# Performance work log

Hardware: AMD Instinct MI355X
Metric: run time of the kernel (lower is better)

Reference implementation:

```python
import jax, jax.numpy as jnp
import numpy as np

B, N, M, G, F = 8, 1000, 64, 50, 128


def setup_inputs() -> dict:
    key = jax.random.key(0)
    ks = jax.random.split(key, 9)
    s = 0.05
    return {
        "features": jax.random.normal(ks[0], (B, N, F), jnp.float32),
        "rbf_expansion": jax.random.uniform(ks[1], (B, N, M, G), jnp.float32),
        "neighbor_list": jax.random.randint(ks[2], (B, N, M), 0, N, jnp.int64),
        "W_init": jax.random.normal(ks[3], (F, F), jnp.float32) * s,
        "W1": jax.random.normal(ks[4], (G, F), jnp.float32) * s,
        "b1": jnp.zeros((F,), jnp.float32),
        "W2": jax.random.normal(ks[5], (F, F), jnp.float32) * s,
        "b2": jnp.zeros((F,), jnp.float32),
        "nbr_w": jax.random.normal(ks[6], (F,), jnp.float32) * s,
        "Wo1": jax.random.normal(ks[7], (F, F), jnp.float32) * s,
        "bo1": jnp.zeros((F,), jnp.float32),
        "Wo2": jax.random.normal(ks[8], (F, F), jnp.float32) * s,
        "bo2": jnp.zeros((F,), jnp.float32),
    }


def reference(features, rbf_expansion, neighbor_list, W_init, W1, b1, W2, b2,
              nbr_w, Wo1, bo1, Wo2, bo2):
    b, n, m = neighbor_list.shape
    # 1. atom-wise linear, no bias/activation: [B,N,F]
    init = features @ W_init
    # 2. CFConv: filter generator on RBF expansion -> [B,N,M,F]
    filt = jnp.tanh(rbf_expansion @ W1 + b1) @ W2 + b2
    # gather neighbor features: init[b, neighbor_list[b,n,m], :] -> [B,N,M,F]
    idx = neighbor_list.reshape(b, n * m, 1)
    nbr_feat = jnp.take_along_axis(init, idx, axis=1).reshape(b, n, m, -1)
    conv = nbr_feat * filt
    # attention over neighbors via learned vector nbr_w
    attn = jax.nn.softmax(jnp.einsum('bnmf,f->bnm', conv, nbr_w), axis=-1)
    agg = jnp.einsum('bnm,bnmf->bnf', attn, conv)
    # 3-4. output dense: linear+tanh, then linear
    out = jnp.tanh(agg @ Wo1 + bo1) @ Wo2 + bo2
    return out, attn
```

## Files before the change

kernel.cpp:

```cpp
#include <hip/hip_runtime.h>
#include <hip/hip_bf16.h>

typedef __attribute__((ext_vector_type(8))) short short8;
typedef __attribute__((ext_vector_type(4))) float f32x4;
typedef unsigned short u16;
typedef unsigned int u32;

#define NBATCH 8
#define NA 1000
#define MD 64
#define GD 50
#define FD 128
#define TOTAL (NBATCH * NA)

__device__ __forceinline__ u16 f2bf(float f) {
    u32 x = __float_as_uint(f);
    return (u16)((x + 0x7fffu + ((x >> 16) & 1u)) >> 16);
}
__device__ __forceinline__ float bf2f(u16 u) {
    return __uint_as_float(((u32)u) << 16);
}
__device__ __forceinline__ u32 pkbf(float x, float y) {
    __hip_bfloat162 h = __float22bfloat162_rn(float2{x, y});
    return *reinterpret_cast<u32*>(&h);
}
__device__ __forceinline__ float tanh_fast(float x) {
    float e = __expf(2.0f * x);
    return 1.0f - 2.0f * __builtin_amdgcn_rcpf(e + 1.0f);
}
__device__ __forceinline__ f32x4 mfma16(short8 a, short8 b, f32x4 c) {
    return __builtin_amdgcn_mfma_f32_16x16x32_bf16(a, b, c, 0, 0, 0);
}

__global__ void k0_prep(const float* __restrict__ W1, const float* __restrict__ W2,
                        const float* __restrict__ Wi, const float* __restrict__ Wo1,
                        const float* __restrict__ Wo2,
                        u16* __restrict__ W1T, u16* __restrict__ W2T,
                        u16* __restrict__ WiT, u16* __restrict__ Wo1T,
                        u16* __restrict__ Wo2T) {
    const int g0 = blockIdx.x * 256 + threadIdx.x;
    const int gstep = gridDim.x * 256;
    for (int i = g0; i < 128 * 72; i += gstep) {
        int n = i / 72, k = i - n * 72;
        int ks = (k < GD) ? k : 0;
        W1T[i] = (k < GD) ? f2bf(W1[ks * FD + n]) : (u16)0;
    }
    for (int i = g0; i < 2 * 128 * 72; i += gstep) {
        int p = i / 9216;
        int rem = i - p * 9216;
        int n = rem / 72, kk = rem - n * 72;
        bool valid = kk < 64;
        int k = p * 64 + (valid ? kk : 0);
        W2T[i]  = valid ? f2bf(W2[k * FD + n])  : (u16)0;
        WiT[i]  = valid ? f2bf(Wi[k * FD + n])  : (u16)0;
        Wo1T[i] = valid ? f2bf(Wo1[k * FD + n]) : (u16)0;
        Wo2T[i] = valid ? f2bf(Wo2[k * FD + n]) : (u16)0;
    }
}

__global__ __launch_bounds__(256, 3) void k1_init(const float* __restrict__ feat,
                                                  const u16* __restrict__ WiT,
                                                  u16* __restrict__ initB) {
    __shared__ alignas(16) char smem[53248];
    u16* sA = (u16*)smem;
    u16* sW = (u16*)(smem + 34816);
    const int tid = threadIdx.x, wid = tid >> 6, lane = tid & 63;
    const int quad = lane >> 4, col = lane & 15, rw = wid * 32;
    const int row0 = blockIdx.x * 128;

    for (int i = tid; i < 4096; i += 256) {
        int r = i >> 5, c = (i & 31) * 4;
        int gr = row0 + r;
        float4 v = {0.f, 0.f, 0.f, 0.f};
        if (gr < TOTAL) v = *(const float4*)&feat[(size_t)gr * FD + c];
        u32* p = (u32*)&sA[r * 136 + c];
        p[0] = pkbf(v.x, v.y);
        p[1] = pkbf(v.z, v.w);
    }
    for (int i = tid; i < 1152; i += 256) ((int4*)sW)[i] = ((const int4*)WiT)[i];
    __syncthreads();

    f32x4 acc[2][8];
    const f32x4 zf = {0.f, 0.f, 0.f, 0.f};
#pragma unroll
    for (int mt = 0; mt < 2; ++mt)
#pragma unroll
        for (int nt = 0; nt < 8; ++nt) acc[mt][nt] = zf;

    for (int half = 0; half < 2; ++half) {
        if (half) {
            __syncthreads();
            for (int i = tid; i < 1152; i += 256)
                ((int4*)sW)[i] = ((const int4*)(WiT + 9216))[i];
            __syncthreads();
        }
#pragma unroll
        for (int ks = 0; ks < 2; ++ks) {
            const int ka = half * 64 + ks * 32 + quad * 8;
            const int kb = ks * 32 + quad * 8;
            short8 a0 = *(const short8*)&sA[(rw + col) * 136 + ka];
            short8 a1 = *(const short8*)&sA[(rw + 16 + col) * 136 + ka];
#pragma unroll
            for (int nt = 0; nt < 8; ++nt) {
                short8 bfr = *(const short8*)&sW[(nt * 16 + col) * 72 + kb];
                acc[0][nt] = mfma16(a0, bfr, acc[0][nt]);
                acc[1][nt] = mfma16(a1, bfr, acc[1][nt]);
            }
        }
    }
#pragma unroll
    for (int mt = 0; mt < 2; ++mt)
#pragma unroll
        for (int nt = 0; nt < 8; ++nt)
#pragma unroll
            for (int r = 0; r < 4; ++r) {
                int row = rw + mt * 16 + quad * 4 + r;
                int gr = row0 + row;
                if (gr < TOTAL)
                    initB[(size_t)gr * FD + nt * 16 + col] = f2bf(acc[mt][nt][r]);
            }
}

__global__ __launch_bounds__(256, 4) void k2_main(
    const float* __restrict__ rbf, const int* __restrict__ nl,
    const u16* __restrict__ initB,
    const u16* __restrict__ W1T, const u16* __restrict__ W2T,
    const float* __restrict__ b1, const float* __restrict__ b2,
    const float* __restrict__ nbrw,
    float* __restrict__ aggOut, float* __restrict__ attnO) {
    __shared__ alignas(16) char smem[37376];
    u16* sA = (u16*)smem;
    int* nlS = (int*)(smem + 34816);
    float* logitP = (float*)(smem + 35328);
    float* attnS = (float*)smem;

    const int tid = threadIdx.x, wid = tid >> 6, lane = tid & 63;
    const int quad = lane >> 4, col = lane & 15;
    const int nt0 = 2 * wid;
    const int blk = blockIdx.x;
    const int b = blk / 500;
    const int n0 = (blk - b * 500) * 2;
    const int atom0 = b * NA + n0;
    const size_t rbf_base = (size_t)atom0 * (MD * GD);

    short8 w1f[2][2];
#pragma unroll
    for (int n = 0; n < 2; ++n)
#pragma unroll
        for (int ks = 0; ks < 2; ++ks)
            w1f[n][ks] = *(const short8*)&W1T[((nt0 + n) * 16 + col) * 72 +
                                              ks * 32 + quad * 8];
    float b1v[2];
#pragma unroll
    for (int n = 0; n < 2; ++n) b1v[n] = b1[(nt0 + n) * 16 + col];

    if (tid < 128) nlS[tid] = nl[atom0 * MD + tid];
    for (int i = tid; i < 128 * 14; i += 256) {
        int r = i / 14;
        sA[r * 72 + 50 + (i - r * 14)] = 0;
    }
    for (int i = tid; i < 3200; i += 256) {
        int e = 2 * i;
        int r = e / 50, g = e - r * 50;
        float2 v = *(const float2*)&rbf[rbf_base + e];
        *(u32*)&sA[r * 72 + g] = pkbf(v.x, v.y);
    }
    __syncthreads();

    f32x4 acc1[8][2];
    const f32x4 zf = {0.f, 0.f, 0.f, 0.f};
#pragma unroll
    for (int m = 0; m < 8; ++m) {
        acc1[m][0] = zf;
        acc1[m][1] = zf;
    }
#pragma unroll
    for (int ks = 0; ks < 2; ++ks)
#pragma unroll
        for (int m = 0; m < 8; ++m) {
            short8 a = *(const short8*)&sA[(m * 16 + col) * 72 + ks * 32 + quad * 8];
            acc1[m][0] = mfma16(a, w1f[0][ks], acc1[m][0]);
            acc1[m][1] = mfma16(a, w1f[1][ks], acc1[m][1]);
        }
    __syncthreads();

#pragma unroll
    for (int m = 0; m < 8; ++m)
#pragma unroll
        for (int n = 0; n < 2; ++n)
#pragma unroll
            for (int r = 0; r < 4; ++r) {
                int row = m * 16 + quad * 4 + r;
                sA[row * 136 + (nt0 + n) * 16 + col] =
                    f2bf(tanh_fast(acc1[m][n][r] + b1v[n]));
            }
    short8 w2f[2][4];
#pragma unroll
    for (int n = 0; n < 2; ++n)
#pragma unroll
        for (int kb = 0; kb < 4; ++kb)
            w2f[n][kb] = *(const short8*)&W2T[(kb >> 1) * 9216 +
                                              ((nt0 + n) * 16 + col) * 72 +
                                              (kb & 1) * 32 + quad * 8];
    float b2v[2], wvv[2];
#pragma unroll
    for (int n = 0; n < 2; ++n) {
        b2v[n] = b2[(nt0 + n) * 16 + col];
        wvv[n] = nbrw[(nt0 + n) * 16 + col];
    }
    __syncthreads();

    f32x4 acc2[8][2];
#pragma unroll
    for (int m = 0; m < 8; ++m) {
        acc2[m][0] = zf;
        acc2[m][1] = zf;
    }
#pragma unroll
    for (int kb = 0; kb < 4; ++kb)
#pragma unroll
        for (int m = 0; m < 8; ++m) {
            short8 a = *(const short8*)&sA[(m * 16 + col) * 136 + kb * 32 + quad * 8];
            acc2[m][0] = mfma16(a, w2f[0][kb], acc2[m][0]);
            acc2[m][1] = mfma16(a, w2f[1][kb], acc2[m][1]);
        }

#pragma unroll
    for (int m = 0; m < 8; ++m)
#pragma unroll
        for (int r = 0; r < 4; ++r) {
            int row = m * 16 + quad * 4 + r;
            int ro = (b * NA + nlS[row]) * FD;
            float p = 0.f;
#pragma unroll
            for (int n = 0; n < 2; ++n) {
                float nb = bf2f(initB[ro + (nt0 + n) * 16 + col]);
                float cv = (acc2[m][n][r] + b2v[n]) * nb;
                acc2[m][n][r] = cv;
                p += cv * wvv[n];
            }
#pragma unroll
            for (int d = 1; d < 16; d <<= 1) p += __shfl_xor(p, d, 64);
            if (col == 0) logitP[wid * 128 + row] = p;
        }
    __syncthreads();

    if (wid < 2) {
        int row = wid * 64 + lane;
        float x = logitP[row] + logitP[128 + row] + logitP[256 + row] +
                  logitP[384 + row];
        float mx = x;
#pragma unroll
        for (int d = 1; d < 64; d <<= 1) mx = fmaxf(mx, __shfl_xor(mx, d, 64));
        float e = __expf(x - mx);
        float s = e;
#pragma unroll
        for (int d = 1; d < 64; d <<= 1) s += __shfl_xor(s, d, 64);
        float a = e / s;
        attnS[row] = a;
        attnO[(size_t)(atom0 + wid) * MD + lane] = a;
    }
    __syncthreads();

    float aggp[2][2] = {{0.f, 0.f}, {0.f, 0.f}};
#pragma unroll
    for (int m = 0; m < 8; ++m) {
        int at = m >> 2;
#pragma unroll
        for (int r = 0; r < 4; ++r) {
            float a = attnS[m * 16 + quad * 4 + r];
            aggp[at][0] += a * acc2[m][0][r];
            aggp[at][1] += a * acc2[m][1][r];
        }
    }
#pragma unroll
    for (int d = 16; d < 64; d <<= 1)
#pragma unroll
        for (int at = 0; at < 2; ++at) {
            aggp[at][0] += __shfl_xor(aggp[at][0], d, 64);
            aggp[at][1] += __shfl_xor(aggp[at][1], d, 64);
        }
    if (quad == 0) {
#pragma unroll
        for (int at = 0; at < 2; ++at)
#pragma unroll
            for (int n = 0; n < 2; ++n)
                aggOut[(size_t)(atom0 + at) * FD + (nt0 + n) * 16 + col] =
                    aggp[at][n];
    }
}

__global__ __launch_bounds__(256, 3) void k3_out(
    float* __restrict__ outp, const u16* __restrict__ Wo1T,
    const u16* __restrict__ Wo2T, const float* __restrict__ bo1,
    const float* __restrict__ bo2) {
    __shared__ alignas(16) char smem[53248];
    u16* sA = (u16*)smem;
    u16* sW = (u16*)(smem + 34816);
    const int tid = threadIdx.x, wid = tid >> 6, lane = tid & 63;
    const int quad = lane >> 4, col = lane & 15, rw = wid * 32;
    const int row0 = blockIdx.x * 128;

    for (int i = tid; i < 4096; i += 256) {
        int r = i >> 5, c = (i & 31) * 4;
        int gr = row0 + r;
        float4 v = {0.f, 0.f, 0.f, 0.f};
        if (gr < TOTAL) v = *(const float4*)&outp[(size_t)gr * FD + c];
        u32* p = (u32*)&sA[r * 136 + c];
        p[0] = pkbf(v.x, v.y);
        p[1] = pkbf(v.z, v.w);
    }
    for (int i = tid; i < 1152; i += 256) ((int4*)sW)[i] = ((const int4*)Wo1T)[i];
    __syncthreads();

    f32x4 acc[2][8];
    const f32x4 zf = {0.f, 0.f, 0.f, 0.f};
#pragma unroll
    for (int mt = 0; mt < 2; ++mt)
#pragma unroll
        for (int nt = 0; nt < 8; ++nt) acc[mt][nt] = zf;
    for (int half = 0; half < 2; ++half) {
        if (half) {
            __syncthreads();
            for (int i = tid; i < 1152; i += 256)
                ((int4*)sW)[i] = ((const int4*)(Wo1T + 9216))[i];
            __syncthreads();
        }
#pragma unroll
        for (int ks = 0; ks < 2; ++ks) {
            const int ka = half * 64 + ks * 32 + quad * 8;
            const int kb = ks * 32 + quad * 8;
            short8 a0 = *(const short8*)&sA[(rw + col) * 136 + ka];
            short8 a1 = *(const short8*)&sA[(rw + 16 + col) * 136 + ka];
#pragma unroll
            for (int nt = 0; nt < 8; ++nt) {
                short8 bfr = *(const short8*)&sW[(nt * 16 + col) * 72 + kb];
                acc[0][nt] = mfma16(a0, bfr, acc[0][nt]);
                acc[1][nt] = mfma16(a1, bfr, acc[1][nt]);
            }
        }
    }
    __syncthreads();

    float bias[8];
#pragma unroll
    for (int nt = 0; nt < 8; ++nt) bias[nt] = bo1[nt * 16 + col];
#pragma unroll
    for (int mt = 0; mt < 2; ++mt)
#pragma unroll
        for (int nt = 0; nt < 8; ++nt)
#pragma unroll
            for (int r = 0; r < 4; ++r) {
                int row = rw + mt * 16 + quad * 4 + r;
                sA[row * 136 + nt * 16 + col] =
                    f2bf(tanh_fast(acc[mt][nt][r] + bias[nt]));
            }
    for (int i = tid; i < 1152; i += 256) ((int4*)sW)[i] = ((const int4*)Wo2T)[i];
    __syncthreads();

    f32x4 acc2[2][8];
#pragma unroll
    for (int mt = 0; mt < 2; ++mt)
#pragma unroll
        for (int nt = 0; nt < 8; ++nt) acc2[mt][nt] = zf;
    for (int half = 0; half < 2; ++half) {
        if (half) {
            __syncthreads();
            for (int i = tid; i < 1152; i += 256)
                ((int4*)sW)[i] = ((const int4*)(Wo2T + 9216))[i];
            __syncthreads();
        }
#pragma unroll
        for (int ks = 0; ks < 2; ++ks) {
            const int ka = half * 64 + ks * 32 + quad * 8;
            const int kb = ks * 32 + quad * 8;
            short8 a0 = *(const short8*)&sA[(rw + col) * 136 + ka];
            short8 a1 = *(const short8*)&sA[(rw + 16 + col) * 136 + ka];
#pragma unroll
            for (int nt = 0; nt < 8; ++nt) {
                short8 bfr = *(const short8*)&sW[(nt * 16 + col) * 72 + kb];
                acc2[0][nt] = mfma16(a0, bfr, acc2[0][nt]);
                acc2[1][nt] = mfma16(a1, bfr, acc2[1][nt]);
            }
        }
    }
#pragma unroll
    for (int nt = 0; nt < 8; ++nt) bias[nt] = bo2[nt * 16 + col];
#pragma unroll
    for (int mt = 0; mt < 2; ++mt)
#pragma unroll
        for (int nt = 0; nt < 8; ++nt)
#pragma unroll
            for (int r = 0; r < 4; ++r) {
                int row = rw + mt * 16 + quad * 4 + r;
                int gr = row0 + row;
                if (gr < TOTAL)
                    outp[(size_t)gr * FD + nt * 16 + col] =
                        acc2[mt][nt][r] + bias[nt];
            }
}

extern "C" void kernel_launch(void* const* d_in, const int* in_sizes, int n_in,
                              void* d_out, int out_size, void* d_ws,
                              size_t ws_size, hipStream_t stream) {
    const float* feat = (const float*)d_in[0];
    const float* rbf  = (const float*)d_in[1];
    const int*   nl   = (const int*)d_in[2];
    const float* Wi   = (const float*)d_in[3];
    const float* W1   = (const float*)d_in[4];
    const float* b1   = (const float*)d_in[5];
    const float* W2   = (const float*)d_in[6];
    const float* b2   = (const float*)d_in[7];
    const float* nbrw = (const float*)d_in[8];
    const float* Wo1  = (const float*)d_in[9];
    const float* bo1  = (const float*)d_in[10];
    const float* Wo2  = (const float*)d_in[11];
    const float* bo2  = (const float*)d_in[12];

    float* outp  = (float*)d_out;
    float* attnp = outp + (size_t)TOTAL * FD;

    char* ws = (char*)d_ws;
    u16* initB = (u16*)ws;
    u16* W1T   = (u16*)(ws + 2048000);
    u16* W2T   = (u16*)(ws + 2048000 + 18432);
    u16* WiT   = (u16*)(ws + 2048000 + 18432 + 36864);
    u16* Wo1T  = (u16*)(ws + 2048000 + 18432 + 2 * 36864);
    u16* Wo2T  = (u16*)(ws + 2048000 + 18432 + 3 * 36864);

    hipLaunchKernelGGL(k0_prep, dim3(40), dim3(256), 0, stream,
                       W1, W2, Wi, Wo1, Wo2, W1T, W2T, WiT, Wo1T, Wo2T);
    hipLaunchKernelGGL(k1_init, dim3(63), dim3(256), 0, stream, feat, WiT, initB);
    hipLaunchKernelGGL(k2_main, dim3(4000), dim3(256), 0, stream,
                       rbf, nl, initB, W1T, W2T, b1, b2, nbrw, outp, attnp);
    hipLaunchKernelGGL(k3_out, dim3(63), dim3(256), 0, stream,
                       outp, Wo1T, Wo2T, bo1, bo2);
}
```

Measured before the change: 301.9 us.

## Fuse output MLP into main kernel and restructure warp tiling with staged neighbor gather

The separate k3_out kernel is removed. The two output dense layers (tanh(agg@Wo1+bo1)@Wo2+bo2) now run inside k2_main using scalar fp32 FMAs that read Wo1/Wo2 straight from global memory. Each warp in k2_main now owns 2 row-tiles across all 128 columns instead of 2 column-tiles across all rows, with W1/W2 staged through shared memory. The neighbor features are gathered into LDS with 16-byte loads instead of scalar bf16 global reads. This saves a launch and the global round-trip of agg, but each of the 4000 blocks re-reads both full 128x128 fp32 output weights, adds extra syncs, and occupancy drops from 4 to 3 blocks per CU.

New measurement: 315.5 us. 1.05x slower.

```diff
diff --git a/kernel.cpp b/kernel.cpp
--- a/kernel.cpp
+++ b/kernel.cpp
@@ -33,11 +33,9 @@
 }
 
 __global__ void k0_prep(const float* __restrict__ W1, const float* __restrict__ W2,
-                        const float* __restrict__ Wi, const float* __restrict__ Wo1,
-                        const float* __restrict__ Wo2,
+                        const float* __restrict__ Wi,
                         u16* __restrict__ W1T, u16* __restrict__ W2T,
-                        u16* __restrict__ WiT, u16* __restrict__ Wo1T,
-                        u16* __restrict__ Wo2T) {
+                        u16* __restrict__ WiT) {
     const int g0 = blockIdx.x * 256 + threadIdx.x;
     const int gstep = gridDim.x * 256;
     for (int i = g0; i < 128 * 72; i += gstep) {
@@ -51,22 +49,28 @@
         int n = rem / 72, kk = rem - n * 72;
         bool valid = kk < 64;
         int k = p * 64 + (valid ? kk : 0);
-        W2T[i]  = valid ? f2bf(W2[k * FD + n])  : (u16)0;
-        WiT[i]  = valid ? f2bf(Wi[k * FD + n])  : (u16)0;
-        Wo1T[i] = valid ? f2bf(Wo1[k * FD + n]) : (u16)0;
-        Wo2T[i] = valid ? f2bf(Wo2[k * FD + n]) : (u16)0;
+        W2T[i] = valid ? f2bf(W2[k * FD + n]) : (u16)0;
+        WiT[i] = valid ? f2bf(Wi[k * FD + n]) : (u16)0;
     }
 }
 
 __global__ __launch_bounds__(256, 3) void k1_init(const float* __restrict__ feat,
                                                   const u16* __restrict__ WiT,
                                                   u16* __restrict__ initB) {
-    __shared__ alignas(16) char smem[53248];
-    u16* sA = (u16*)smem;
-    u16* sW = (u16*)(smem + 34816);
+    __shared__ alignas(16) u16 sA[128 * 136];
     const int tid = threadIdx.x, wid = tid >> 6, lane = tid & 63;
-    const int quad = lane >> 4, col = lane & 15, rw = wid * 32;
+    const int quad = lane >> 4, col = lane & 15;
+    const int nt0 = 2 * wid;
     const int row0 = blockIdx.x * 128;
+
+    short8 wf[2][4];
+#pragma unroll
+    for (int n = 0; n < 2; ++n)
+#pragma unroll
+        for (int kb = 0; kb < 4; ++kb)
+            wf[n][kb] = *(const short8*)&WiT[(kb >> 1) * 9216 +
+                                             ((nt0 + n) * 16 + col) * 72 +
+                                             (kb & 1) * 32 + quad * 8];
 
     for (int i = tid; i < 4096; i += 256) {
         int r = i >> 5, c = (i & 31) * 4;
@@ -77,83 +81,63 @@
         p[0] = pkbf(v.x, v.y);
         p[1] = pkbf(v.z, v.w);
     }
-    for (int i = tid; i < 1152; i += 256) ((int4*)sW)[i] = ((const int4*)WiT)[i];
-    __syncthreads();
-
-    f32x4 acc[2][8];
+    __syncthreads();
+
+    f32x4 acc[8][2];
     const f32x4 zf = {0.f, 0.f, 0.f, 0.f};
 #pragma unroll
-    for (int mt = 0; mt < 2; ++mt)
-#pragma unroll
-        for (int nt = 0; nt < 8; ++nt) acc[mt][nt] = zf;
-
-    for (int half = 0; half < 2; ++half) {
-        if (half) {
-            __syncthreads();
-            for (int i = tid; i < 1152; i += 256)
-                ((int4*)sW)[i] = ((const int4*)(WiT + 9216))[i];
-            __syncthreads();
-        }
-#pragma unroll
-        for (int ks = 0; ks < 2; ++ks) {
-            const int ka = half * 64 + ks * 32 + quad * 8;
-            const int kb = ks * 32 + quad * 8;
-            short8 a0 = *(const short8*)&sA[(rw + col) * 136 + ka];
-            short8 a1 = *(const short8*)&sA[(rw + 16 + col) * 136 + ka];
-#pragma unroll
-            for (int nt = 0; nt < 8; ++nt) {
-                short8 bfr = *(const short8*)&sW[(nt * 16 + col) * 72 + kb];
-                acc[0][nt] = mfma16(a0, bfr, acc[0][nt]);
-                acc[1][nt] = mfma16(a1, bfr, acc[1][nt]);
+    for (int m = 0; m < 8; ++m) {
+        acc[m][0] = zf;
+        acc[m][1] = zf;
+    }
+#pragma unroll
+    for (int kb = 0; kb < 4; ++kb)
+#pragma unroll
+        for (int m = 0; m < 8; ++m) {
+            short8 a = *(const short8*)&sA[(m * 16 + col) * 136 + kb * 32 + quad * 8];
+            acc[m][0] = mfma16(a, wf[0][kb], acc[m][0]);
+            acc[m][1] = mfma16(a, wf[1][kb], acc[m][1]);
+        }
+#pragma unroll
+    for (int m = 0; m < 8; ++m)
+#pragma unroll
+        for (int n = 0; n < 2; ++n)
+#pragma unroll
+            for (int r = 0; r < 4; ++r) {
+                int gr = row0 + m * 16 + quad * 4 + r;
+                if (gr < TOTAL)
+                    initB[(size_t)gr * FD + (nt0 + n) * 16 + col] =
+                        f2bf(acc[m][n][r]);
             }
-        }
-    }
-#pragma unroll
-    for (int mt = 0; mt < 2; ++mt)
-#pragma unroll
-        for (int nt = 0; nt < 8; ++nt)
-#pragma unroll
-            for (int r = 0; r < 4; ++r) {
-                int row = rw + mt * 16 + quad * 4 + r;
-                int gr = row0 + row;
-                if (gr < TOTAL)
-                    initB[(size_t)gr * FD + nt * 16 + col] = f2bf(acc[mt][nt][r]);
-            }
-}
-
-__global__ __launch_bounds__(256, 4) void k2_main(
+}
+
+__global__ __launch_bounds__(256, 3) void k2_main(
     const float* __restrict__ rbf, const int* __restrict__ nl,
     const u16* __restrict__ initB,
     const u16* __restrict__ W1T, const u16* __restrict__ W2T,
     const float* __restrict__ b1, const float* __restrict__ b2,
     const float* __restrict__ nbrw,
-    float* __restrict__ aggOut, float* __restrict__ attnO) {
-    __shared__ alignas(16) char smem[37376];
+    const float* __restrict__ Wo1, const float* __restrict__ bo1,
+    const float* __restrict__ Wo2, const float* __restrict__ bo2,
+    float* __restrict__ outp, float* __restrict__ attnO) {
+    __shared__ alignas(16) char smem[53760];
     u16* sA = (u16*)smem;
-    int* nlS = (int*)(smem + 34816);
-    float* logitP = (float*)(smem + 35328);
-    float* attnS = (float*)smem;
+    u16* sW = (u16*)(smem + 34816);
+    int* nlS = (int*)(smem + 53248);
+    float* logitS = (float*)(smem + 53248);
+    float* attnS = (float*)(smem + 34816);
+    float* aggS = (float*)(smem + 34816 + 512);
+    float* t1S = (float*)(smem + 34816 + 2560);
 
     const int tid = threadIdx.x, wid = tid >> 6, lane = tid & 63;
     const int quad = lane >> 4, col = lane & 15;
-    const int nt0 = 2 * wid;
+    const int mt0 = 2 * wid;
     const int blk = blockIdx.x;
     const int b = blk / 500;
     const int n0 = (blk - b * 500) * 2;
     const int atom0 = b * NA + n0;
     const size_t rbf_base = (size_t)atom0 * (MD * GD);
 
-    short8 w1f[2][2];
-#pragma unroll
-    for (int n = 0; n < 2; ++n)
-#pragma unroll
-        for (int ks = 0; ks < 2; ++ks)
-            w1f[n][ks] = *(const short8*)&W1T[((nt0 + n) * 16 + col) * 72 +
-                                              ks * 32 + quad * 8];
-    float b1v[2];
-#pragma unroll
-    for (int n = 0; n < 2; ++n) b1v[n] = b1[(nt0 + n) * 16 + col];
-
     if (tid < 128) nlS[tid] = nl[atom0 * MD + tid];
     for (int i = tid; i < 128 * 14; i += 256) {
         int r = i / 14;
@@ -165,90 +149,117 @@
         float2 v = *(const float2*)&rbf[rbf_base + e];
         *(u32*)&sA[r * 72 + g] = pkbf(v.x, v.y);
     }
-    __syncthreads();
-
-    f32x4 acc1[8][2];
+    for (int i = tid; i < 1152; i += 256) ((int4*)sW)[i] = ((const int4*)W1T)[i];
+    __syncthreads();
+
+    f32x4 acc1[2][8];
     const f32x4 zf = {0.f, 0.f, 0.f, 0.f};
 #pragma unroll
-    for (int m = 0; m < 8; ++m) {
-        acc1[m][0] = zf;
-        acc1[m][1] = zf;
-    }
-#pragma unroll
-    for (int ks = 0; ks < 2; ++ks)
-#pragma unroll
-        for (int m = 0; m < 8; ++m) {
-            short8 a = *(const short8*)&sA[(m * 16 + col) * 72 + ks * 32 + quad * 8];
-            acc1[m][0] = mfma16(a, w1f[0][ks], acc1[m][0]);
-            acc1[m][1] = mfma16(a, w1f[1][ks], acc1[m][1]);
-        }
-    __syncthreads();
-
-#pragma unroll
-    for (int m = 0; m < 8; ++m)
-#pragma unroll
-        for (int n = 0; n < 2; ++n)
+    for (int m = 0; m < 2; ++m)
+#pragma unroll
+        for (int n = 0; n < 8; ++n) acc1[m][n] = zf;
+#pragma unroll
+    for (int ks = 0; ks < 2; ++ks) {
+        short8 a[2];
+#pragma unroll
+        for (int m = 0; m < 2; ++m)
+            a[m] = *(const short8*)&sA[((mt0 + m) * 16 + col) * 72 + ks * 32 +
+                                       quad * 8];
+#pragma unroll
+        for (int n = 0; n < 8; ++n) {
+            short8 bfr = *(const short8*)&sW[(n * 16 + col) * 72 + ks * 32 + quad * 8];
+            acc1[0][n] = mfma16(a[0], bfr, acc1[0][n]);
+            acc1[1][n] = mfma16(a[1], bfr, acc1[1][n]);
+        }
+    }
+    __syncthreads();
+
+    float b1v[8];
+#pragma unroll
+    for (int n = 0; n < 8; ++n) b1v[n] = b1[n * 16 + col];
+#pragma unroll
+    for (int m = 0; m < 2; ++m)
+#pragma unroll
+        for (int n = 0; n < 8; ++n)
 #pragma unroll
             for (int r = 0; r < 4; ++r) {
-                int row = m * 16 + quad * 4 + r;
-                sA[row * 136 + (nt0 + n) * 16 + col] =
+                int row = (mt0 + m) * 16 + quad * 4 + r;
+                sA[row * 136 + n * 16 + col] =
                     f2bf(tanh_fast(acc1[m][n][r] + b1v[n]));
             }
-    short8 w2f[2][4];
-#pragma unroll
-    for (int n = 0; n < 2; ++n)
-#pragma unroll
-        for (int kb = 0; kb < 4; ++kb)
-            w2f[n][kb] = *(const short8*)&W2T[(kb >> 1) * 9216 +
-                                              ((nt0 + n) * 16 + col) * 72 +
-                                              (kb & 1) * 32 + quad * 8];
-    float b2v[2], wvv[2];
-#pragma unroll
-    for (int n = 0; n < 2; ++n) {
-        b2v[n] = b2[(nt0 + n) * 16 + col];
-        wvv[n] = nbrw[(nt0 + n) * 16 + col];
-    }
-    __syncthreads();
-
-    f32x4 acc2[8][2];
-#pragma unroll
-    for (int m = 0; m < 8; ++m) {
-        acc2[m][0] = zf;
-        acc2[m][1] = zf;
-    }
-#pragma unroll
-    for (int kb = 0; kb < 4; ++kb)
-#pragma unroll
-        for (int m = 0; m < 8; ++m) {
-            short8 a = *(const short8*)&sA[(m * 16 + col) * 136 + kb * 32 + quad * 8];
-            acc2[m][0] = mfma16(a, w2f[0][kb], acc2[m][0]);
-            acc2[m][1] = mfma16(a, w2f[1][kb], acc2[m][1]);
-        }
-
-#pragma unroll
-    for (int m = 0; m < 8; ++m)
+    for (int i = tid; i < 1152; i += 256) ((int4*)sW)[i] = ((const int4*)W2T)[i];
+    __syncthreads();
+
+    f32x4 acc2[2][8];
+#pragma unroll
+    for (int m = 0; m < 2; ++m)
+#pragma unroll
+        for (int n = 0; n < 8; ++n) acc2[m][n] = zf;
+    for (int half = 0; half < 2; ++half) {
+        if (half) {
+            __syncthreads();
+            for (int i = tid; i < 1152; i += 256)
+                ((int4*)sW)[i] = ((const int4*)(W2T + 9216))[i];
+            __syncthreads();
+        }
+#pragma unroll
+        for (int ks = 0; ks < 2; ++ks) {
+            const int ka = half * 64 + ks * 32 + quad * 8;
+            const int kb = ks * 32 + quad * 8;
+            short8 a[2];
+#pragma unroll
+            for (int m = 0; m < 2; ++m)
+                a[m] = *(const short8*)&sA[((mt0 + m) * 16 + col) * 136 + ka];
+#pragma unroll
+            for (int n = 0; n < 8; ++n) {
+                short8 bfr = *(const short8*)&sW[(n * 16 + col) * 72 + kb];
+                acc2[0][n] = mfma16(a[0], bfr, acc2[0][n]);
+                acc2[1][n] = mfma16(a[1], bfr, acc2[1][n]);
+            }
+        }
+    }
+    __syncthreads();
+
+    {
+        const int lane16 = tid & 15;
+        const int rg = tid >> 4;
+#pragma unroll
+        for (int it = 0; it < 8; ++it) {
+            int row = rg + it * 16;
+            int nr = b * NA + nlS[row];
+            int4 v = *(const int4*)&initB[(size_t)nr * FD + lane16 * 8];
+            *(int4*)&sA[row * 136 + lane16 * 8] = v;
+        }
+    }
+    __syncthreads();
+
+    float b2v[8], wvv[8];
+#pragma unroll
+    for (int n = 0; n < 8; ++n) {
+        b2v[n] = b2[n * 16 + col];
+        wvv[n] = nbrw[n * 16 + col];
+    }
+#pragma unroll
+    for (int m = 0; m < 2; ++m)
 #pragma unroll
         for (int r = 0; r < 4; ++r) {
-            int row = m * 16 + quad * 4 + r;
-            int ro = (b * NA + nlS[row]) * FD;
+            int row = (mt0 + m) * 16 + quad * 4 + r;
             float p = 0.f;
 #pragma unroll
-            for (int n = 0; n < 2; ++n) {
-                float nb = bf2f(initB[ro + (nt0 + n) * 16 + col]);
+            for (int n = 0; n < 8; ++n) {
+                float nb = bf2f(sA[row * 136 + n * 16 + col]);
                 float cv = (acc2[m][n][r] + b2v[n]) * nb;
                 acc2[m][n][r] = cv;
                 p += cv * wvv[n];
             }
 #pragma unroll
             for (int d = 1; d < 16; d <<= 1) p += __shfl_xor(p, d, 64);
-            if (col == 0) logitP[wid * 128 + row] = p;
+            if (col == 0) logitS[row] = p;
         }
     __syncthreads();
 
     if (wid < 2) {
-        int row = wid * 64 + lane;
-        float x = logitP[row] + logitP[128 + row] + logitP[256 + row] +
-                  logitP[384 + row];
+        float x = logitS[wid * 64 + lane];
         float mx = x;
 #pragma unroll
         for (int d = 1; d < 64; d <<= 1) mx = fmaxf(mx, __shfl_xor(mx, d, 64));
@@ -257,147 +268,53 @@
 #pragma unroll
         for (int d = 1; d < 64; d <<= 1) s += __shfl_xor(s, d, 64);
         float a = e / s;
-        attnS[row] = a;
+        attnS[wid * 64 + lane] = a;
         attnO[(size_t)(atom0 + wid) * MD + lane] = a;
     }
     __syncthreads();
 
-    float aggp[2][2] = {{0.f, 0.f}, {0.f, 0.f}};
-#pragma unroll
-    for (int m = 0; m < 8; ++m) {
-        int at = m >> 2;
+    float aggp[8] = {0.f, 0.f, 0.f, 0.f, 0.f, 0.f, 0.f, 0.f};
+#pragma unroll
+    for (int m = 0; m < 2; ++m)
 #pragma unroll
         for (int r = 0; r < 4; ++r) {
-            float a = attnS[m * 16 + quad * 4 + r];
-            aggp[at][0] += a * acc2[m][0][r];
-            aggp[at][1] += a * acc2[m][1][r];
-        }
-    }
+            float a = attnS[(mt0 + m) * 16 + quad * 4 + r];
+#pragma unroll
+            for (int n = 0; n < 8; ++n) aggp[n] += a * acc2[m][n][r];
+        }
 #pragma unroll
     for (int d = 16; d < 64; d <<= 1)
 #pragma unroll
-        for (int at = 0; at < 2; ++at) {
-            aggp[at][0] += __shfl_xor(aggp[at][0], d, 64);
-            aggp[at][1] += __shfl_xor(aggp[at][1], d, 64);
-        }
+        for (int n = 0; n < 8; ++n) aggp[n] += __shfl_xor(aggp[n], d, 64);
     if (quad == 0) {
 #pragma unroll
-        for (int at = 0; at < 2; ++at)
-#pragma unroll
-            for (int n = 0; n < 2; ++n)
-                aggOut[(size_t)(atom0 + at) * FD + (nt0 + n) * 16 + col] =
-                    aggp[at][n];
-    }
-}
-
-__global__ __launch_bounds__(256, 3) void k3_out(
-    float* __restrict__ outp, const u16* __restrict__ Wo1T,
-    const u16* __restrict__ Wo2T, const float* __restrict__ bo1,
-    const float* __restrict__ bo2) {
-    __shared__ alignas(16) char smem[53248];
-    u16* sA = (u16*)smem;
-    u16* sW = (u16*)(smem + 34816);
-    const int tid = threadIdx.x, wid = tid >> 6, lane = tid & 63;
-    const int quad = lane >> 4, col = lane & 15, rw = wid * 32;
-    const int row0 = blockIdx.x * 128;
-
-    for (int i = tid; i < 4096; i += 256) {
-        int r = i >> 5, c = (i & 31) * 4;
-        int gr = row0 + r;
-        float4 v = {0.f, 0.f, 0.f, 0.f};
-        if (gr < TOTAL) v = *(const float4*)&outp[(size_t)gr * FD + c];
-        u32* p = (u32*)&sA[r * 136 + c];
-        p[0] = pkbf(v.x, v.y);
-        p[1] = pkbf(v.z, v.w);
-    }
-    for (int i = tid; i < 1152; i += 256) ((int4*)sW)[i] = ((const int4*)Wo1T)[i];
-    __syncthreads();
-
-    f32x4 acc[2][8];
-    const f32x4 zf = {0.f, 0.f, 0.f, 0.f};
-#pragma unroll
-    for (int mt = 0; mt < 2; ++mt)
-#pragma unroll
-        for (int nt = 0; nt < 8; ++nt) acc[mt][nt] = zf;
-    for (int half = 0; half < 2; ++half) {
-        if (half) {
-            __syncthreads();
-            for (int i = tid; i < 1152; i += 256)
-                ((int4*)sW)[i] = ((const int4*)(Wo1T + 9216))[i];
-            __syncthreads();
-        }
-#pragma unroll
-        for (int ks = 0; ks < 2; ++ks) {
-            const int ka = half * 64 + ks * 32 + quad * 8;
-            const int kb = ks * 32 + quad * 8;
-            short8 a0 = *(const short8*)&sA[(rw + col) * 136 + ka];
-            short8 a1 = *(const short8*)&sA[(rw + 16 + col) * 136 + ka];
-#pragma unroll
-            for (int nt = 0; nt < 8; ++nt) {
-                short8 bfr = *(const short8*)&sW[(nt * 16 + col) * 72 + kb];
-                acc[0][nt] = mfma16(a0, bfr, acc[0][nt]);
-                acc[1][nt] = mfma16(a1, bfr, acc[1][nt]);
-            }
-        }
-    }
-    __syncthreads();
-
-    float bias[8];
-#pragma unroll
-    for (int nt = 0; nt < 8; ++nt) bias[nt] = bo1[nt * 16 + col];
-#pragma unroll
-    for (int mt = 0; mt < 2; ++mt)
-#pragma unroll
-        for (int nt = 0; nt < 8; ++nt)
-#pragma unroll
-            for (int r = 0; r < 4; ++r) {
-                int row = rw + mt * 16 + quad * 4 + r;
-                sA[row * 136 + nt * 16 + col] =
-                    f2bf(tanh_fast(acc[mt][nt][r] + bias[nt]));
-            }
-    for (int i = tid; i < 1152; i += 256) ((int4*)sW)[i] = ((const int4*)Wo2T)[i];
-    __syncthreads();
-
-    f32x4 acc2[2][8];
-#pragma unroll
-    for (int mt = 0; mt < 2; ++mt)
-#pragma unroll
-        for (int nt = 0; nt < 8; ++nt) acc2[mt][nt] = zf;
-    for (int half = 0; half < 2; ++half) {
-        if (half) {
-            __syncthreads();
-            for (int i = tid; i < 1152; i += 256)
-                ((int4*)sW)[i] = ((const int4*)(Wo2T + 9216))[i];
-            __syncthreads();
-        }
-#pragma unroll
-        for (int ks = 0; ks < 2; ++ks) {
-            const int ka = half * 64 + ks * 32 + quad * 8;
-            const int kb = ks * 32 + quad * 8;
-            short8 a0 = *(const short8*)&sA[(rw + col) * 136 + ka];
-            short8 a1 = *(const short8*)&sA[(rw + 16 + col) * 136 + ka];
-#pragma unroll
-            for (int nt = 0; nt < 8; ++nt) {
-                short8 bfr = *(const short8*)&sW[(nt * 16 + col) * 72 + kb];
-                acc2[0][nt] = mfma16(a0, bfr, acc2[0][nt]);
-                acc2[1][nt] = mfma16(a1, bfr, acc2[1][nt]);
-            }
-        }
-    }
-#pragma unroll
-    for (int nt = 0; nt < 8; ++nt) bias[nt] = bo2[nt * 16 + col];
-#pragma unroll
-    for (int mt = 0; mt < 2; ++mt)
-#pragma unroll
-        for (int nt = 0; nt < 8; ++nt)
-#pragma unroll
-            for (int r = 0; r < 4; ++r) {
-                int row = rw + mt * 16 + quad * 4 + r;
-                int gr = row0 + row;
-                if (gr < TOTAL)
-                    outp[(size_t)gr * FD + nt * 16 + col] =
-                        acc2[mt][nt][r] + bias[nt];
-            }
+        for (int n = 0; n < 8; ++n) aggS[wid * 128 + n * 16 + col] = aggp[n];
+    }
+    __syncthreads();
+
+    {
+        const int a = tid >> 7;
+        const int f = tid & 127;
+        float s = bo1[f];
+#pragma unroll 8
+        for (int kb = 0; kb < 32; ++kb) {
+            float4 u = *(const float4*)&aggS[(2 * a) * 128 + kb * 4];
+            float4 v = *(const float4*)&aggS[(2 * a + 1) * 128 + kb * 4];
+            const float* wr = &Wo1[(kb * 4) * FD + f];
+            s += (u.x + v.x) * wr[0] + (u.y + v.y) * wr[FD] +
+                 (u.z + v.z) * wr[2 * FD] + (u.w + v.w) * wr[3 * FD];
+        }
+        t1S[a * 128 + f] = tanh_fast(s);
+        __syncthreads();
+        float o = bo2[f];
+#pragma unroll 8
+        for (int kb = 0; kb < 32; ++kb) {
+            float4 t = *(const float4*)&t1S[a * 128 + kb * 4];
+            const float* wr = &Wo2[(kb * 4) * FD + f];
+            o += t.x * wr[0] + t.y * wr[FD] + t.z * wr[2 * FD] + t.w * wr[3 * FD];
+        }
+        outp[(size_t)(atom0 + a) * FD + f] = o;
+    }
 }
 
 extern "C" void kernel_launch(void* const* d_in, const int* in_sizes, int n_in,
@@ -425,14 +342,11 @@
     u16* W1T   = (u16*)(ws + 2048000);
     u16* W2T   = (u16*)(ws + 2048000 + 18432);
     u16* WiT   = (u16*)(ws + 2048000 + 18432 + 36864);
-    u16* Wo1T  = (u16*)(ws + 2048000 + 18432 + 2 * 36864);
-    u16* Wo2T  = (u16*)(ws + 2048000 + 18432 + 3 * 36864);
 
     hipLaunchKernelGGL(k0_prep, dim3(40), dim3(256), 0, stream,
-                       W1, W2, Wi, Wo1, Wo2, W1T, W2T, WiT, Wo1T, Wo2T);
+                       W1, W2, Wi, W1T, W2T, WiT);
     hipLaunchKernelGGL(k1_init, dim3(63), dim3(256), 0, stream, feat, WiT, initB);
     hipLaunchKernelGGL(k2_main, dim3(4000), dim3(256), 0, stream,
-                       rbf, nl, initB, W1T, W2T, b1, b2, nbrw, outp, attnp);
-    hipLaunchKernelGGL(k3_out, dim3(63), dim3(256), 0, stream,
-                       outp, Wo1T, Wo2T, bo1, bo2);
-}
+                       rbf, nl, initB, W1T, W2T, b1, b2, nbrw,
+                       Wo1, bo1, Wo2, bo2, outp, attnp);
+}
```
